# Performance work log

Hardware: AMD Instinct MI355X
Metric: run time of the kernel (lower is better)

Reference implementation:

```python
import jax, jax.numpy as jnp
import numpy as np

N_QUBITS = 12
FAST_DEPTH = 4
FAST_DECAY = 0.9
LATENT = 512
BATCH = 2048


def _apply_ry(state, theta, wire):
    # state: (B, 2**n) real; RY is a real rotation. PennyLane default.qubit:
    # wire 0 is the most-significant bit of the state index.
    B = state.shape[0]
    s = state.reshape(B, 1 << wire, 2, -1)
    h = theta * 0.5
    c = jnp.cos(h)[:, None, None]
    sn = jnp.sin(h)[:, None, None]
    s0, s1 = s[:, :, 0], s[:, :, 1]
    out = jnp.stack([c * s0 - sn * s1, sn * s0 + c * s1], axis=2)
    return out.reshape(state.shape)


def _apply_cnot_adjacent(state, wire):
    # CNOT with control=wire, target=wire+1 (nearest-neighbor chain)
    B = state.shape[0]
    s = state.reshape(B, 1 << wire, 2, 2, -1)
    out = jnp.stack([s[:, :, 0], s[:, :, 1, ::-1]], axis=2)
    return out.reshape(state.shape)


def _fwp_circuit(x, fast, n_qubits, n_outputs):
    # x: (B, n_qubits) RY encoding angles; fast: (B, depth, n_qubits)
    B = x.shape[0]
    dim = 1 << n_qubits
    # Hadamard layer on |0...0> -> uniform positive real amplitudes.
    state = jnp.full((B, dim), 2.0 ** (-n_qubits / 2), dtype=x.dtype)
    for w in range(n_qubits):
        state = _apply_ry(state, x[:, w], w)
    for layer in range(fast.shape[1]):
        for w in range(n_qubits - 1):
            state = _apply_cnot_adjacent(state, w)
        for w in range(n_qubits):
            state = _apply_ry(state, fast[:, layer, w], w)
    probs = state * state  # real state -> |amp|^2
    outs = []
    for w in range(n_outputs):
        p = probs.reshape(B, 1 << w, 2, -1)
        outs.append(p[:, :, 0].sum(axis=(1, 2)) - p[:, :, 1].sum(axis=(1, 2)))
    return jnp.stack(outs, axis=1)  # (B, n_outputs) PauliZ expvals


def setup_inputs() -> dict:
    key = jax.random.key(0)
    ks = jax.random.split(key, 6)
    n, depth, latent = N_QUBITS, FAST_DEPTH, LATENT
    return {
        "x_t": jax.random.normal(ks[0], (BATCH, n), jnp.float32),
        "fast_prev": jax.random.normal(ks[1], (BATCH, depth, n), jnp.float32) * 0.1,
        "W_enc": jax.random.normal(ks[2], (latent, n), jnp.float32) / np.sqrt(n).astype(np.float32),
        "b_enc": jnp.zeros((latent,), jnp.float32),
        "W_upd": jax.random.normal(ks[3], (depth * n, latent), jnp.float32) / np.sqrt(latent).astype(np.float32),
        "b_upd": jnp.zeros((depth * n,), jnp.float32),
        "W_ro": jax.random.normal(ks[4], (1, n), jnp.float32) / np.sqrt(n).astype(np.float32),
        "b_ro": jnp.zeros((1,), jnp.float32),
    }


def reference(x_t, fast_prev, W_enc, b_enc, W_upd, b_upd, W_ro, b_ro):
    latent = jnp.tanh(x_t @ W_enc.T + b_enc)
    delta = (latent @ W_upd.T + b_upd).reshape(x_t.shape[0], FAST_DEPTH, N_QUBITS)
    fast_next = FAST_DECAY * fast_prev + delta
    q_out = _fwp_circuit(x_t, fast_next, N_QUBITS, N_QUBITS)  # n_outputs = n_qubits
    y_t = q_out @ W_ro.T + b_ro
    return (y_t, fast_next)
```

## Files before the change

### kernel.cpp

```cpp
#include <hip/hip_runtime.h>

static constexpr int NQ    = 12;
static constexpr int DEPTH = 4;
static constexpr int LAT   = 512;
static constexpr int FAST  = DEPTH * NQ;
static constexpr float DECAY = 0.9f;

using v2f = __attribute__((ext_vector_type(2))) float;


__device__ __forceinline__ constexpr int G6(int x){ return (x ^ (x >> 1)) & 63; }

__device__ __forceinline__ float bperm(int idx, float v){
    return __int_as_float(__builtin_amdgcn_ds_bpermute(idx, __float_as_int(v)));
}
template<int CTRL>
__device__ __forceinline__ float dppf(float x){
    return __int_as_float(__builtin_amdgcn_mov_dpp(__float_as_int(x), CTRL, 0xF, 0xF, false));
}
template<int CTRL>
__device__ __forceinline__ v2f dpp2(v2f v){ return (v2f){dppf<CTRL>(v.x), dppf<CTRL>(v.y)}; }

__device__ __forceinline__ float xsum32(float x){
    float a = x, b = x;
    asm("v_permlane32_swap_b32 %0, %1" : "+v"(a), "+v"(b));
    return a + b;
}
__device__ __forceinline__ float xsum16(float x){
    float a = x, b = x;
    asm("v_permlane16_swap_b32 %0, %1" : "+v"(a), "+v"(b));
    return a + b;
}

template<int S>
__device__ __forceinline__ void rw(v2f (&u)[64], v2f cc, v2f ss){
    #pragma unroll
    for (int r = 0; r < 64; r++){
        if (!(r & S)){
            v2f a = u[r], b = u[r | S];
            u[r]     = cc * a - ss * b;
            u[r | S] = ss * a + cc * b;
        }
    }
}

__global__ __launch_bounds__(64, 1)
void fwp_kernel(const float* __restrict__ x_t,
                const float* __restrict__ fast_prev,
                const float* __restrict__ W_enc,
                const float* __restrict__ b_enc,
                const float* __restrict__ W_upd,
                const float* __restrict__ b_upd,
                const float* __restrict__ W_ro,
                const float* __restrict__ b_ro,
                float* __restrict__ out_y,
                float* __restrict__ out_fast) {
    const int lane = threadIdx.x;
    const int eA   = 2 * blockIdx.x;
    const int eB   = eA + 1;

    __shared__ __align__(16) float latA[LAT], latB[LAT];
    __shared__ __align__(8)  v2f CC[FAST], SS[FAST];

    float xaA[NQ], xaB[NQ];
    #pragma unroll
    for (int k = 0; k < NQ; k++) {
        xaA[k] = x_t[eA * NQ + k];
        xaB[k] = x_t[eB * NQ + k];
    }

    {
        const float4* we = (const float4*)(W_enc + lane * 8 * NQ);
        float4 be0 = *(const float4*)&b_enc[8 * lane];
        float4 be1 = *(const float4*)&b_enc[8 * lane + 4];
        float be[8] = {be0.x, be0.y, be0.z, be0.w, be1.x, be1.y, be1.z, be1.w};
        float lA[8], lB[8];
        #pragma unroll
        for (int t = 0; t < 8; t++) {
            float4 a0 = we[3 * t], a1 = we[3 * t + 1], a2 = we[3 * t + 2];
            float sA = be[t]
                + a0.x * xaA[0] + a0.y * xaA[1] + a0.z * xaA[2]  + a0.w * xaA[3]
                + a1.x * xaA[4] + a1.y * xaA[5] + a1.z * xaA[6]  + a1.w * xaA[7]
                + a2.x * xaA[8] + a2.y * xaA[9] + a2.z * xaA[10] + a2.w * xaA[11];
            float sB = be[t]
                + a0.x * xaB[0] + a0.y * xaB[1] + a0.z * xaB[2]  + a0.w * xaB[3]
                + a1.x * xaB[4] + a1.y * xaB[5] + a1.z * xaB[6]  + a1.w * xaB[7]
                + a2.x * xaB[8] + a2.y * xaB[9] + a2.z * xaB[10] + a2.w * xaB[11];
            lA[t] = tanhf(sA);
            lB[t] = tanhf(sB);
        }
        *(float4*)&latA[8 * lane]     = (float4){lA[0], lA[1], lA[2], lA[3]};
        *(float4*)&latA[8 * lane + 4] = (float4){lA[4], lA[5], lA[6], lA[7]};
        *(float4*)&latB[8 * lane]     = (float4){lB[0], lB[1], lB[2], lB[3]};
        *(float4*)&latB[8 * lane + 4] = (float4){lB[4], lB[5], lB[6], lB[7]};
    }

    if (lane < FAST) {
        const float4* wr = (const float4*)(W_upd + lane * LAT);
        const float4* la = (const float4*)(latA);
        const float4* lb = (const float4*)(latB);
        float base = b_upd[lane];
        float sA = base, sB = base;
        #pragma unroll 8
        for (int j = 0; j < LAT / 4; j++) {
            float4 w4 = wr[j];
            float4 a4 = la[j];
            float4 b4 = lb[j];
            sA += w4.x * a4.x + w4.y * a4.y + w4.z * a4.z + w4.w * a4.w;
            sB += w4.x * b4.x + w4.y * b4.y + w4.z * b4.z + w4.w * b4.w;
        }
        float angA = DECAY * fast_prev[eA * FAST + lane] + sA;
        float angB = DECAY * fast_prev[eB * FAST + lane] + sB;
        out_fast[eA * FAST + lane] = angA;
        out_fast[eB * FAST + lane] = angB;
        CC[lane] = (v2f){__cosf(0.5f * angA), __cosf(0.5f * angB)};
        SS[lane] = (v2f){__sinf(0.5f * angA), __sinf(0.5f * angB)};
    }

    v2f u[64];
    {
        v2f g0[NQ], g1[NQ];
        #pragma unroll
        for (int w = 0; w < NQ; w++) {
            float hA = 0.5f * xaA[w], hB = 0.5f * xaB[w];
            float cA = __cosf(hA), sA = __sinf(hA);
            float cB = __cosf(hB), sB = __sinf(hB);
            const float K = 0.70710678118654752f;
            g0[w] = (v2f){(cA - sA) * K, (cB - sB) * K};
            g1[w] = (v2f){(cA + sA) * K, (cB + sB) * K};
        }
        v2f L = (v2f){1.0f, 1.0f};
        #pragma unroll
        for (int w = 6; w < NQ; w++)
            L *= ((lane >> (11 - w)) & 1) ? g1[w] : g0[w];
        u[0] = L;
        #pragma unroll
        for (int w = 0; w < 6; w++) {
            const int S = 32 >> w;
            #pragma unroll
            for (int r = 0; r < 64; r += 2 * S) {
                u[r + S] = u[r] * g1[w];
                u[r]     = u[r] * g0[w];
            }
        }
    }

    const int idxA = G6(lane) * 4;
    const int idxB = idxA ^ 128;

    #define SIG1(h, src) { const int idx_ = ((h) & 1) ? idxB : idxA; \
        u[h] = (v2f){ bperm(idx_, (src).x), bperm(idx_, (src).y) }; }

    #pragma unroll 1
    for (int layer = 0; layer < DEPTH; layer++) {
        v2f cc[NQ], ss[NQ];
        #pragma unroll
        for (int w = 0; w < NQ; w++) { cc[w] = CC[layer * NQ + w]; ss[w] = SS[layer * NQ + w]; }

        SIG1(0, u[0]);  SIG1(1, u[1]);
        { v2f t = u[2]; SIG1(2, u[3]); SIG1(3, t); }
        { v2f t = u[4]; SIG1(4, u[6]);  SIG1(6, u[5]);  SIG1(5, u[7]);  SIG1(7, t); }
        { v2f t = u[8]; SIG1(8, u[12]); SIG1(12, u[10]); SIG1(10, u[15]); SIG1(15, t); }
        { v2f t = u[9]; SIG1(9, u[13]); SIG1(13, u[11]); SIG1(11, u[14]); SIG1(14, t); }
        { v2f t = u[16]; SIG1(16, u[24]); SIG1(24, u[20]); SIG1(20, u[30]); SIG1(30, u[17]);
                         SIG1(17, u[25]); SIG1(25, u[21]); SIG1(21, u[31]); SIG1(31, t); }
        { v2f t = u[18]; SIG1(18, u[27]); SIG1(27, u[22]); SIG1(22, u[29]); SIG1(29, u[19]);
                         SIG1(19, u[26]); SIG1(26, u[23]); SIG1(23, u[28]); SIG1(28, t); }
        { v2f t = u[32]; SIG1(32, u[48]); SIG1(48, u[40]); SIG1(40, u[60]); SIG1(60, u[34]);
                         SIG1(34, u[51]); SIG1(51, u[42]); SIG1(42, u[63]); SIG1(63, t); }
        { v2f t = u[33]; SIG1(33, u[49]); SIG1(49, u[41]); SIG1(41, u[61]); SIG1(61, u[35]);
                         SIG1(35, u[50]); SIG1(50, u[43]); SIG1(43, u[62]); SIG1(62, t); }
        { v2f t = u[36]; SIG1(36, u[54]); SIG1(54, u[45]); SIG1(45, u[59]); SIG1(59, u[38]);
                         SIG1(38, u[53]); SIG1(53, u[47]); SIG1(47, u[56]); SIG1(56, t); }
        { v2f t = u[37]; SIG1(37, u[55]); SIG1(55, u[44]); SIG1(44, u[58]); SIG1(58, u[39]);
                         SIG1(39, u[52]); SIG1(52, u[46]); SIG1(46, u[57]); SIG1(57, t); }

        {
            v2f sv = (lane & 32) ? ss[6] : -ss[6];
            v2f cm = cc[6] - sv;
            #pragma unroll
            for (int h = 0; h < 64; h++) {
                v2f s2 = (v2f){ xsum32(u[h].x), xsum32(u[h].y) };
                u[h] = cm * u[h] + sv * s2;
            }
        }
        {
            v2f sv = (lane & 16) ? ss[7] : -ss[7];
            v2f cm = cc[7] - sv;
            #pragma unroll
            for (int h = 0; h < 64; h++) {
                v2f s2 = (v2f){ xsum16(u[h].x), xsum16(u[h].y) };
                u[h] = cm * u[h] + sv * s2;
            }
        }
        {
            v2f sv = (lane & 8) ? ss[8] : -ss[8];
            #pragma unroll
            for (int h = 0; h < 64; h++) {
                v2f p = dpp2<0x128>(u[h]);
                u[h] = cc[8] * u[h] + sv * p;
            }
        }
        {
            v2f sv = (lane & 4) ? ss[9] : -ss[9];
            #pragma unroll
            for (int h = 0; h < 64; h++) {
                v2f p = dpp2<0x141>(dpp2<0x1B>(u[h]));
                u[h] = cc[9] * u[h] + sv * p;
            }
        }
        {
            v2f sv = (lane & 2) ? ss[10] : -ss[10];
            #pragma unroll
            for (int h = 0; h < 64; h++) {
                v2f p = dpp2<0x4E>(u[h]);
                u[h] = cc[10] * u[h] + sv * p;
            }
        }
        {
            v2f sv = (lane & 1) ? ss[11] : -ss[11];
            #pragma unroll
            for (int h = 0; h < 64; h++) {
                v2f p = dpp2<0xB1>(u[h]);
                u[h] = cc[11] * u[h] + sv * p;
            }
        }
        rw<32>(u, cc[0], ss[0]);
        rw<16>(u, cc[1], ss[1]);
        rw<8> (u, cc[2], ss[2]);
        rw<4> (u, cc[3], ss[3]);
        rw<2> (u, cc[4], ss[4]);
        rw<1> (u, cc[5], ss[5]);
    }
    #undef SIG1

    float wro[NQ];
    #pragma unroll
    for (int w = 0; w < NQ; w++) wro[w] = W_ro[w];
    float sl = 0.0f;
    #pragma unroll
    for (int w = 6; w < NQ; w++)
        sl += ((lane >> (11 - w)) & 1) ? -wro[w] : wro[w];

    v2f tot = (v2f){0.0f, 0.0f};
    v2f pw[6];
    #pragma unroll
    for (int k = 0; k < 6; k++) pw[k] = (v2f){0.0f, 0.0f};
    #pragma unroll
    for (int r = 0; r < 64; r++) {
        v2f p = u[r] * u[r];
        tot += p;
        pw[0] += (r & 32) ? -p : p;
        pw[1] += (r & 16) ? -p : p;
        pw[2] += (r & 8)  ? -p : p;
        pw[3] += (r & 4)  ? -p : p;
        pw[4] += (r & 2)  ? -p : p;
        pw[5] += (r & 1)  ? -p : p;
    }
    v2f y2 = (v2f){sl, sl} * tot;
    #pragma unroll
    for (int k = 0; k < 6; k++) y2 += (v2f){wro[k], wro[k]} * pw[k];
    float yA = y2.x, yB = y2.y;
    #pragma unroll
    for (int m = 32; m >= 1; m >>= 1) {
        yA += __shfl_xor(yA, m, 64);
        yB += __shfl_xor(yB, m, 64);
    }
    if (lane == 0) {
        float br = b_ro[0];
        out_y[eA] = yA + br;
        out_y[eB] = yB + br;
    }
}

extern "C" void kernel_launch(void* const* d_in, const int* in_sizes, int n_in,
                              void* d_out, int out_size, void* d_ws, size_t ws_size,
                              hipStream_t stream) {
    const float* x_t       = (const float*)d_in[0];
    const float* fast_prev = (const float*)d_in[1];
    const float* W_enc     = (const float*)d_in[2];
    const float* b_enc     = (const float*)d_in[3];
    const float* W_upd     = (const float*)d_in[4];
    const float* b_upd     = (const float*)d_in[5];
    const float* W_ro      = (const float*)d_in[6];
    const float* b_ro      = (const float*)d_in[7];
    float* out = (float*)d_out;

    fwp_kernel<<<1024, 64, 0, stream>>>(x_t, fast_prev, W_enc, b_enc,
                                        W_upd, b_upd, W_ro, b_ro,
                                        out , out + 2048 );
}
```

Baseline: 114.3 us.

## Split angle computation into separate wide kernel before circuit simulation kernel

Moves the encoder MLP, update projection and cos/sin generation out of the 64-thread circuit kernel into its own kernel with 256 threads per block handling four batch elements. The angle kernel writes cos/sin pairs to the workspace, and the circuit kernel loads them into shared memory. This aims to stop the single-wave circuit blocks from idling on the serial 512-long dot products, and gives the angle work more parallelism through split accumulators. The cost is an extra kernel launch and a global-memory round trip for the cos/sin table.

```diff
diff --git a/kernel.cpp b/kernel.cpp
--- a/kernel.cpp
+++ b/kernel.cpp
@@ -44,77 +44,93 @@
     }
 }
 
-__global__ __launch_bounds__(64, 1)
-void fwp_kernel(const float* __restrict__ x_t,
+__global__ __launch_bounds__(256, 1)
+void fwp_angles(const float* __restrict__ x_t,
                 const float* __restrict__ fast_prev,
                 const float* __restrict__ W_enc,
                 const float* __restrict__ b_enc,
                 const float* __restrict__ W_upd,
                 const float* __restrict__ b_upd,
-                const float* __restrict__ W_ro,
-                const float* __restrict__ b_ro,
-                float* __restrict__ out_y,
-                float* __restrict__ out_fast) {
+                float* __restrict__ out_fast,
+                float2* __restrict__ cs_out) {
+    const int t  = threadIdx.x;
+    const int e0 = blockIdx.x * 4;
+
+    __shared__ __align__(16) float lat[4][LAT];
+    __shared__ float xs[4 * NQ];
+
+    if (t < 4 * NQ) xs[t] = x_t[e0 * NQ + t];
+    __syncthreads();
+
+    {
+        const int ee = t >> 6;
+        float xr[NQ];
+        #pragma unroll
+        for (int m = 0; m < NQ; m++) xr[m] = xs[ee * NQ + m];
+        #pragma unroll
+        for (int k = 0; k < 8; k++) {
+            const int j = (t & 63) | (k << 6);
+            const float4* wr = (const float4*)(W_enc + j * NQ);
+            float4 a0 = wr[0], a1 = wr[1], a2 = wr[2];
+            float s = b_enc[j]
+                + a0.x * xr[0] + a0.y * xr[1] + a0.z * xr[2]  + a0.w * xr[3]
+                + a1.x * xr[4] + a1.y * xr[5] + a1.z * xr[6]  + a1.w * xr[7]
+                + a2.x * xr[8] + a2.y * xr[9] + a2.z * xr[10] + a2.w * xr[11];
+            lat[ee][j] = tanhf(s);
+        }
+    }
+    __syncthreads();
+
+    if (t < 4 * FAST) {
+        const int ee = t / FAST;
+        const int w  = t - ee * FAST;
+        const float4* wr = (const float4*)(W_upd + w * LAT);
+        const float4* la = (const float4*)(&lat[ee][0]);
+        float s0 = 0.f, s1 = 0.f, s2 = 0.f, s3 = 0.f;
+        #pragma unroll 8
+        for (int j = 0; j < LAT / 4; j += 4) {
+            float4 w0 = wr[j],     l0 = la[j];
+            float4 w1 = wr[j + 1], l1 = la[j + 1];
+            float4 w2 = wr[j + 2], l2 = la[j + 2];
+            float4 w3 = wr[j + 3], l3 = la[j + 3];
+            s0 += w0.x * l0.x + w0.y * l0.y + w0.z * l0.z + w0.w * l0.w;
+            s1 += w1.x * l1.x + w1.y * l1.y + w1.z * l1.z + w1.w * l1.w;
+            s2 += w2.x * l2.x + w2.y * l2.y + w2.z * l2.z + w2.w * l2.w;
+            s3 += w3.x * l3.x + w3.y * l3.y + w3.z * l3.z + w3.w * l3.w;
+        }
+        const int e   = e0 + ee;
+        const int off = e * FAST + w;
+        float ang = DECAY * fast_prev[off] + (b_upd[w] + ((s0 + s1) + (s2 + s3)));
+        out_fast[off] = ang;
+        float h = 0.5f * ang;
+        cs_out[off] = (float2){__cosf(h), __sinf(h)};
+    }
+}
+
+__global__ __launch_bounds__(64, 1)
+void fwp_circuit(const float* __restrict__ x_t,
+                 const float2* __restrict__ cs_in,
+                 const float* __restrict__ W_ro,
+                 const float* __restrict__ b_ro,
+                 float* __restrict__ out_y) {
     const int lane = threadIdx.x;
     const int eA   = 2 * blockIdx.x;
     const int eB   = eA + 1;
 
-    __shared__ __align__(16) float latA[LAT], latB[LAT];
-    __shared__ __align__(8)  v2f CC[FAST], SS[FAST];
+    __shared__ __align__(8) v2f CC[FAST], SS[FAST];
+
+    if (lane < FAST) {
+        float2 a = cs_in[eA * FAST + lane];
+        float2 b = cs_in[eB * FAST + lane];
+        CC[lane] = (v2f){a.x, b.x};
+        SS[lane] = (v2f){a.y, b.y};
+    }
 
     float xaA[NQ], xaB[NQ];
     #pragma unroll
     for (int k = 0; k < NQ; k++) {
         xaA[k] = x_t[eA * NQ + k];
         xaB[k] = x_t[eB * NQ + k];
-    }
-
-    {
-        const float4* we = (const float4*)(W_enc + lane * 8 * NQ);
-        float4 be0 = *(const float4*)&b_enc[8 * lane];
-        float4 be1 = *(const float4*)&b_enc[8 * lane + 4];
-        float be[8] = {be0.x, be0.y, be0.z, be0.w, be1.x, be1.y, be1.z, be1.w};
-        float lA[8], lB[8];
-        #pragma unroll
-        for (int t = 0; t < 8; t++) {
-            float4 a0 = we[3 * t], a1 = we[3 * t + 1], a2 = we[3 * t + 2];
-            float sA = be[t]
-                + a0.x * xaA[0] + a0.y * xaA[1] + a0.z * xaA[2]  + a0.w * xaA[3]
-                + a1.x * xaA[4] + a1.y * xaA[5] + a1.z * xaA[6]  + a1.w * xaA[7]
-                + a2.x * xaA[8] + a2.y * xaA[9] + a2.z * xaA[10] + a2.w * xaA[11];
-            float sB = be[t]
-                + a0.x * xaB[0] + a0.y * xaB[1] + a0.z * xaB[2]  + a0.w * xaB[3]
-                + a1.x * xaB[4] + a1.y * xaB[5] + a1.z * xaB[6]  + a1.w * xaB[7]
-                + a2.x * xaB[8] + a2.y * xaB[9] + a2.z * xaB[10] + a2.w * xaB[11];
-            lA[t] = tanhf(sA);
-            lB[t] = tanhf(sB);
-        }
-        *(float4*)&latA[8 * lane]     = (float4){lA[0], lA[1], lA[2], lA[3]};
-        *(float4*)&latA[8 * lane + 4] = (float4){lA[4], lA[5], lA[6], lA[7]};
-        *(float4*)&latB[8 * lane]     = (float4){lB[0], lB[1], lB[2], lB[3]};
-        *(float4*)&latB[8 * lane + 4] = (float4){lB[4], lB[5], lB[6], lB[7]};
-    }
-
-    if (lane < FAST) {
-        const float4* wr = (const float4*)(W_upd + lane * LAT);
-        const float4* la = (const float4*)(latA);
-        const float4* lb = (const float4*)(latB);
-        float base = b_upd[lane];
-        float sA = base, sB = base;
-        #pragma unroll 8
-        for (int j = 0; j < LAT / 4; j++) {
-            float4 w4 = wr[j];
-            float4 a4 = la[j];
-            float4 b4 = lb[j];
-            sA += w4.x * a4.x + w4.y * a4.y + w4.z * a4.z + w4.w * a4.w;
-            sB += w4.x * b4.x + w4.y * b4.y + w4.z * b4.z + w4.w * b4.w;
-        }
-        float angA = DECAY * fast_prev[eA * FAST + lane] + sA;
-        float angB = DECAY * fast_prev[eB * FAST + lane] + sB;
-        out_fast[eA * FAST + lane] = angA;
-        out_fast[eB * FAST + lane] = angB;
-        CC[lane] = (v2f){__cosf(0.5f * angA), __cosf(0.5f * angB)};
-        SS[lane] = (v2f){__sinf(0.5f * angA), __sinf(0.5f * angB)};
     }
 
     v2f u[64];
@@ -285,8 +301,10 @@
     const float* W_ro      = (const float*)d_in[6];
     const float* b_ro      = (const float*)d_in[7];
     float* out = (float*)d_out;
-
-    fwp_kernel<<<1024, 64, 0, stream>>>(x_t, fast_prev, W_enc, b_enc,
-                                        W_upd, b_upd, W_ro, b_ro,
-                                        out , out + 2048 );
-}
+    float2* cs_tab = (float2*)d_ws;
+
+    fwp_angles<<<512, 256, 0, stream>>>(x_t, fast_prev, W_enc, b_enc,
+                                        W_upd, b_upd,
+                                        out + 2048 , cs_tab);
+    fwp_circuit<<<1024, 64, 0, stream>>>(x_t, cs_tab, W_ro, b_ro, out );
+}
```

New measurement: 126.6 us. 1.11x slower.
